# Optimization experiments

Hardware: AMD Instinct MI355X
Metric: run time of the kernel (lower is better)

Reference implementation:

```python
import jax, jax.numpy as jnp
import numpy as np

D = 2048
H = 16
DH = D // H  # 128
B = 512
EPS = 1e-5


def _layernorm(x, g, b):
    m = jnp.mean(x, axis=-1, keepdims=True)
    v = jnp.mean((x - m) ** 2, axis=-1, keepdims=True)
    return (x - m) * jax.lax.rsqrt(v + EPS) * g + b


def setup_inputs() -> dict:
    key = jax.random.key(0)
    ks = jax.random.split(key, 16)
    s_in = 1.0 / np.sqrt(D)
    s_ff = 1.0 / np.sqrt(4 * D)
    return {
        "x": jax.random.normal(ks[0], (B, D), jnp.float32),
        # per-head q/k/v projections, stacked over heads: [H, D, DH]
        "Wq": jax.random.uniform(ks[1], (H, D, DH), jnp.float32, -s_in, s_in),
        "bq": jax.random.uniform(ks[2], (H, DH), jnp.float32, -s_in, s_in),
        "Wk": jax.random.uniform(ks[3], (H, D, DH), jnp.float32, -s_in, s_in),
        "bk": jax.random.uniform(ks[4], (H, DH), jnp.float32, -s_in, s_in),
        "Wv": jax.random.uniform(ks[5], (H, D, DH), jnp.float32, -s_in, s_in),
        "bv": jax.random.uniform(ks[6], (H, DH), jnp.float32, -s_in, s_in),
        "Wo": jax.random.uniform(ks[7], (D, D), jnp.float32, -s_in, s_in),
        "bo": jax.random.uniform(ks[8], (D,), jnp.float32, -s_in, s_in),
        "W1": jax.random.uniform(ks[9], (D, 4 * D), jnp.float32, -s_in, s_in),
        "b1": jax.random.uniform(ks[10], (4 * D,), jnp.float32, -s_in, s_in),
        "W2": jax.random.uniform(ks[11], (4 * D, D), jnp.float32, -s_ff, s_ff),
        "b2": jax.random.uniform(ks[12], (D,), jnp.float32, -s_ff, s_ff),
        "g1": jnp.ones((D,), jnp.float32),
        "be1": jnp.zeros((D,), jnp.float32),
        "g2": jnp.ones((D,), jnp.float32),
        "be2": jnp.zeros((D,), jnp.float32),
    }


def reference(x, Wq, bq, Wk, bk, Wv, bv, Wo, bo, W1, b1, W2, b2, g1, be1, g2, be2):
    # --- pre-norm attention branch ---
    h = _layernorm(x, g1, be1)                       # [B, D]
    q = jnp.einsum('bd,hde->bhe', h, Wq) + bq        # [B, H, DH]
    k = jnp.einsum('bd,hde->bhe', h, Wk) + bk
    v = jnp.einsum('bd,hde->bhe', h, Wv) + bv
    # outer-product 'attention' per sample: [B, H, DH, DH]
    attn = q[..., :, None] * k[..., None, :] / jnp.sqrt(jnp.float32(DH))
    attn = jax.nn.softmax(attn, axis=-1)
    o = jnp.einsum('bhij,bhj->bhi', attn, v)         # [B, H, DH]
    o = o.reshape(x.shape[0], H * DH)                # concat over heads
    x = x + o @ Wo + bo
    # --- pre-norm FFN branch ---
    h2 = _layernorm(x, g2, be2)
    x = x + jax.nn.relu(h2 @ W1 + b1) @ W2 + b2
    return x
```

## Files before the change

### kernel.cpp

```cpp
#include <hip/hip_runtime.h>
#include <hip/hip_bf16.h>
#include <math.h>


#define DDIM 2048
#define HHEADS 16
#define DHEAD 128
#define BROWS 512
#define LN_EPS 1e-5f

typedef __bf16 bf16x8_t __attribute__((ext_vector_type(8)));
typedef float f32x4_t __attribute__((ext_vector_type(4)));

#define GLD16(gptr, lptr)                                                     \
    __builtin_amdgcn_global_load_lds(                                         \
        (const __attribute__((address_space(1))) void*)(gptr),                \
        (__attribute__((address_space(3))) void*)(lptr), 16, 0, 0)

__global__ __launch_bounds__(256) void ln_kernel(const float* __restrict__ x,
                                                 const float* __restrict__ g,
                                                 const float* __restrict__ b,
                                                 __bf16* __restrict__ out) {
    const int row = blockIdx.x;
    const int tid = threadIdx.x;
    const float4* x4 = (const float4*)(x + (size_t)row * DDIM);
    float4 a = x4[2 * tid];
    float4 c = x4[2 * tid + 1];
    float s  = a.x + a.y + a.z + a.w + c.x + c.y + c.z + c.w;
    float s2 = a.x*a.x + a.y*a.y + a.z*a.z + a.w*a.w
             + c.x*c.x + c.y*c.y + c.z*c.z + c.w*c.w;
    #pragma unroll
    for (int off = 32; off > 0; off >>= 1) {
        s  += __shfl_down(s, off);
        s2 += __shfl_down(s2, off);
    }
    __shared__ float ps[4], ps2[4];
    __shared__ float mean_s, rstd_s;
    const int lane = tid & 63, w = tid >> 6;
    if (lane == 0) { ps[w] = s; ps2[w] = s2; }
    __syncthreads();
    if (tid == 0) {
        float S  = ps[0] + ps[1] + ps[2] + ps[3];
        float S2 = ps2[0] + ps2[1] + ps2[2] + ps2[3];
        float m  = S * (1.0f / DDIM);
        float var = S2 * (1.0f / DDIM) - m * m;
        mean_s = m;
        rstd_s = rsqrtf(var + LN_EPS);
    }
    __syncthreads();
    const float m = mean_s, r = rstd_s;
    const float4* g4 = (const float4*)g;
    const float4* b4 = (const float4*)b;
    float4 ga = g4[2 * tid], gb = g4[2 * tid + 1];
    float4 ba = b4[2 * tid], bb = b4[2 * tid + 1];
    bf16x8_t o;
    o[0] = (__bf16)((a.x - m) * r * ga.x + ba.x);
    o[1] = (__bf16)((a.y - m) * r * ga.y + ba.y);
    o[2] = (__bf16)((a.z - m) * r * ga.z + ba.z);
    o[3] = (__bf16)((a.w - m) * r * ga.w + ba.w);
    o[4] = (__bf16)((c.x - m) * r * gb.x + bb.x);
    o[5] = (__bf16)((c.y - m) * r * gb.y + bb.y);
    o[6] = (__bf16)((c.z - m) * r * gb.z + bb.z);
    o[7] = (__bf16)((c.w - m) * r * gb.w + bb.w);
    *(bf16x8_t*)(out + (size_t)row * DDIM + tid * 8) = o;
}

__global__ __launch_bounds__(256) void transpose_kernel(
    const float* __restrict__ src, __bf16* __restrict__ dst, int R, int C) {
    __shared__ float tile[64][65];
    const size_t bofs = (size_t)blockIdx.z * R * C;
    src += bofs;
    dst += bofs;
    const int c0 = blockIdx.x * 64, r0 = blockIdx.y * 64;
    const int t = threadIdx.x;
    const int rr = t >> 4, cc = (t & 15) * 4;
    #pragma unroll
    for (int p = 0; p < 4; p++) {
        const float4 v =
            *(const float4*)(src + (size_t)(r0 + rr + 16 * p) * C + c0 + cc);
        tile[rr + 16 * p][cc]     = v.x;
        tile[rr + 16 * p][cc + 1] = v.y;
        tile[rr + 16 * p][cc + 2] = v.z;
        tile[rr + 16 * p][cc + 3] = v.w;
    }
    __syncthreads();
    const int slot = t & 7;
    #pragma unroll
    for (int p = 0; p < 2; p++) {
        const int c = (t >> 3) + 32 * p;
        bf16x8_t o;
        #pragma unroll
        for (int j = 0; j < 8; j++)
            o[j] = (__bf16)tile[slot * 8 + j][c];
        *(bf16x8_t*)(dst + (size_t)(c0 + c) * R + r0 + slot * 8) = o;
    }
}

__global__ __launch_bounds__(256) void transpose_qkv_kernel(
    const float* __restrict__ Wq, const float* __restrict__ Wk,
    const float* __restrict__ Wv, __bf16* __restrict__ dstall) {
    __shared__ float tile[64][65];
    const int z = blockIdx.z, which = z >> 4, hd = z & 15;
    const float* src = (which == 0) ? Wq : (which == 1) ? Wk : Wv;
    src += (size_t)hd * DDIM * DHEAD;
    __bf16* dst = dstall + (size_t)which * DDIM * DDIM + (size_t)hd * DDIM * DHEAD;
    const int R = DDIM, C = DHEAD;
    const int c0 = blockIdx.x * 64, r0 = blockIdx.y * 64;
    const int t = threadIdx.x;
    const int rr = t >> 4, cc = (t & 15) * 4;
    #pragma unroll
    for (int p = 0; p < 4; p++) {
        const float4 v =
            *(const float4*)(src + (size_t)(r0 + rr + 16 * p) * C + c0 + cc);
        tile[rr + 16 * p][cc]     = v.x;
        tile[rr + 16 * p][cc + 1] = v.y;
        tile[rr + 16 * p][cc + 2] = v.z;
        tile[rr + 16 * p][cc + 3] = v.w;
    }
    __syncthreads();
    const int slot = t & 7;
    #pragma unroll
    for (int p = 0; p < 2; p++) {
        const int c = (t >> 3) + 32 * p;
        bf16x8_t o;
        #pragma unroll
        for (int j = 0; j < 8; j++)
            o[j] = (__bf16)tile[slot * 8 + j][c];
        *(bf16x8_t*)(dst + (size_t)(c0 + c) * R + r0 + slot * 8) = o;
    }
}

template <int DEPTH, int SPLITZ, int OUT_BF16, int RELU, int RES, int BIAS3>
__global__ __launch_bounds__(512) void gemm_bt(
    const __bf16* __restrict__ A, int K,
    const __bf16* __restrict__ Bt,
    const float* __restrict__ bias, const float* __restrict__ biasB,
    const float* __restrict__ biasC,
    const float* __restrict__ Res,
    void* __restrict__ Cout, int N) {
    constexpr int TM = 128, TN = 128;
    constexpr int STG = (TM + TN) * 64;
    __shared__ __align__(16) __bf16 smem[DEPTH * STG];

    const int tid = threadIdx.x;
    const int w = tid >> 6, lane = tid & 63;
    const int m0 = blockIdx.y * TM, n0 = blockIdx.x * TN;

    const int Kloc = K / SPLITZ;
    const int kb = blockIdx.z * Kloc;
    const int NK = Kloc / 64;

    constexpr int NT = (TM + TN) / 8;
    constexpr int NI = NT / 8;

    const int srow = lane >> 3;
    const int sslot = (lane & 7) ^ srow;

    const __bf16* srcs[NI];
    int toff[NI];
    #pragma unroll
    for (int i = 0; i < NI; i++) {
        const int t = w + 8 * i;
        toff[i] = t * 512;
        const int r = t * 8 + srow;
        srcs[i] = (r < TM)
                      ? A + (size_t)(m0 + r) * K + kb + sslot * 8
                      : Bt + (size_t)(n0 + r - TM) * K + kb + sslot * 8;
    }

    constexpr int MI = 4, NJ = 4;
    const int wg = w & 3, kh = w >> 2;
    const int wm = (wg >> 1) * 64, wn = (wg & 1) * 64;
    const int fm = lane & 15, quad = lane >> 4;
    const int f7 = fm & 7;

    const int sl = ((kh * 4 + quad) ^ f7) * 16;
    int aoff[MI], boff[NJ];
    #pragma unroll
    for (int i = 0; i < MI; i++)
        aoff[i] = (wm + 16 * i + fm) * 128 + sl;
    #pragma unroll
    for (int j = 0; j < NJ; j++)
        boff[j] = (TM + wn + 16 * j + fm) * 128 + sl;

    f32x4_t acc[MI][NJ] = {};

    #pragma unroll
    for (int d = 0; d < DEPTH; d++)
        #pragma unroll
        for (int i = 0; i < NI; i++)
            GLD16(srcs[i] + d * 64, smem + d * STG + toff[i]);

    for (int ks = 0; ks < NK; ks++) {
        const char* st = (const char*)smem + (ks % DEPTH) * (STG * 2);
        asm volatile("s_waitcnt vmcnt(%0)\n\ts_barrier"
                     :: "i"((DEPTH - 1) * NI) : "memory");

        bf16x8_t a[MI], b[NJ];
        #pragma unroll
        for (int i = 0; i < MI; i++)
            a[i] = *(const bf16x8_t*)(st + aoff[i]);
        #pragma unroll
        for (int j = 0; j < NJ; j++)
            b[j] = *(const bf16x8_t*)(st + boff[j]);
        #pragma unroll
        for (int i = 0; i < MI; i++)
            #pragma unroll
            for (int j = 0; j < NJ; j++)
                acc[i][j] = __builtin_amdgcn_mfma_f32_16x16x32_bf16(
                    a[i], b[j], acc[i][j], 0, 0, 0);

        asm volatile("s_waitcnt lgkmcnt(0)\n\ts_barrier" ::: "memory");
        if (ks + DEPTH < NK) {
            __bf16* dst = smem + (ks % DEPTH) * STG;
            #pragma unroll
            for (int i = 0; i < NI; i++)
                GLD16(srcs[i] + (size_t)(ks + DEPTH) * 64, dst + toff[i]);
        }
    }

    char* mrg = (char*)smem + wg * 16384;
    if (kh == 1) {
        #pragma unroll
        for (int i = 0; i < MI; i++)
            #pragma unroll
            for (int j = 0; j < NJ; j++)
                *(f32x4_t*)(mrg + (((i * NJ + j) * 64) + lane) * 16) = acc[i][j];
    }
    __syncthreads();
    if (kh == 1) return;
    #pragma unroll
    for (int i = 0; i < MI; i++)
        #pragma unroll
        for (int j = 0; j < NJ; j++) {
            const f32x4_t p = *(const f32x4_t*)(mrg + (((i * NJ + j) * 64) + lane) * 16);
            acc[i][j][0] += p[0]; acc[i][j][1] += p[1];
            acc[i][j][2] += p[2]; acc[i][j][3] += p[3];
        }

    if (SPLITZ > 1) {
        float* P = (float*)Cout + (size_t)blockIdx.z * (gridDim.y * TM) * N;
        #pragma unroll
        for (int i = 0; i < MI; i++)
            #pragma unroll
            for (int j = 0; j < NJ; j++) {
                const int col = n0 + wn + 16 * j + fm;
                #pragma unroll
                for (int r = 0; r < 4; r++) {
                    const int row = m0 + wm + 16 * i + quad * 4 + r;
                    P[(size_t)row * N + col] = acc[i][j][r];
                }
            }
    } else {
        const float* bp = bias;
        if (BIAS3) {
            const int seg = n0 >> 11;
            bp = (seg == 0) ? bias : (seg == 1) ? biasB : biasC;
        }
        #pragma unroll
        for (int i = 0; i < MI; i++)
            #pragma unroll
            for (int j = 0; j < NJ; j++) {
                const int col = n0 + wn + 16 * j + fm;
                const float bcol = BIAS3 ? bp[col & 2047] : bp[col];
                #pragma unroll
                for (int r = 0; r < 4; r++) {
                    const int row = m0 + wm + 16 * i + quad * 4 + r;
                    float val = acc[i][j][r] + bcol;
                    if (RES) val += Res[(size_t)row * N + col];
                    if (RELU) val = fmaxf(val, 0.0f);
                    if (OUT_BF16)
                        ((__bf16*)Cout)[(size_t)row * N + col] = (__bf16)val;
                    else
                        ((float*)Cout)[(size_t)row * N + col] = val;
                }
            }
    }
}

template <int NS>
__global__ __launch_bounds__(256) void reduce_splitk(
    const float* __restrict__ part, const float* __restrict__ Res,
    const float* __restrict__ bias, float* __restrict__ out) {
    const int idx = blockIdx.x * 256 + threadIdx.x;
    const float4 b4 = ((const float4*)bias)[idx & 511];
    float4 r = ((const float4*)Res)[idx];
    #pragma unroll
    for (int s = 0; s < NS; s++) {
        const float4 p = ((const float4*)part)[(size_t)s * 262144 + idx];
        r.x += p.x; r.y += p.y; r.z += p.z; r.w += p.w;
    }
    r.x += b4.x; r.y += b4.y; r.z += b4.z; r.w += b4.w;
    ((float4*)out)[idx] = r;
}

template <int NS>
__global__ __launch_bounds__(256) void reduce_ln_kernel(
    const float* __restrict__ part, const float* __restrict__ x,
    const float* __restrict__ bo, const float* __restrict__ g,
    const float* __restrict__ be, float* __restrict__ x1,
    __bf16* __restrict__ h2) {
    const int row = blockIdx.x;
    const int tid = threadIdx.x;
    const size_t rbase = (size_t)row * DDIM;
    float v[8];
    #pragma unroll
    for (int p = 0; p < 2; p++) {
        const int c = tid * 8 + p * 4;
        float4 r = *(const float4*)(x + rbase + c);
        const float4 b4 = *(const float4*)(bo + c);
        r.x += b4.x; r.y += b4.y; r.z += b4.z; r.w += b4.w;
        #pragma unroll
        for (int s = 0; s < NS; s++) {
            const float4 q = *(const float4*)(part + (size_t)s * BROWS * DDIM + rbase + c);
            r.x += q.x; r.y += q.y; r.z += q.z; r.w += q.w;
        }
        *(float4*)(x1 + rbase + c) = r;
        v[p * 4 + 0] = r.x; v[p * 4 + 1] = r.y; v[p * 4 + 2] = r.z; v[p * 4 + 3] = r.w;
    }
    float s = 0.f, s2 = 0.f;
    #pragma unroll
    for (int i = 0; i < 8; i++) { s += v[i]; s2 += v[i] * v[i]; }
    #pragma unroll
    for (int off = 32; off > 0; off >>= 1) {
        s  += __shfl_down(s, off);
        s2 += __shfl_down(s2, off);
    }
    __shared__ float ps[4], ps2[4];
    __shared__ float mean_s, rstd_s;
    const int lane = tid & 63, wv = tid >> 6;
    if (lane == 0) { ps[wv] = s; ps2[wv] = s2; }
    __syncthreads();
    if (tid == 0) {
        float S  = ps[0] + ps[1] + ps[2] + ps[3];
        float S2 = ps2[0] + ps2[1] + ps2[2] + ps2[3];
        float m  = S * (1.0f / DDIM);
        float var = S2 * (1.0f / DDIM) - m * m;
        mean_s = m;
        rstd_s = rsqrtf(var + LN_EPS);
    }
    __syncthreads();
    const float m = mean_s, r = rstd_s;
    const float4* g4 = (const float4*)g;
    const float4* b4 = (const float4*)be;
    float4 ga = g4[2 * tid], gb = g4[2 * tid + 1];
    float4 ba = b4[2 * tid], bb = b4[2 * tid + 1];
    bf16x8_t o;
    o[0] = (__bf16)((v[0] - m) * r * ga.x + ba.x);
    o[1] = (__bf16)((v[1] - m) * r * ga.y + ba.y);
    o[2] = (__bf16)((v[2] - m) * r * ga.z + ba.z);
    o[3] = (__bf16)((v[3] - m) * r * ga.w + ba.w);
    o[4] = (__bf16)((v[4] - m) * r * gb.x + bb.x);
    o[5] = (__bf16)((v[5] - m) * r * gb.y + bb.y);
    o[6] = (__bf16)((v[6] - m) * r * gb.z + bb.z);
    o[7] = (__bf16)((v[7] - m) * r * gb.w + bb.w);
    *(bf16x8_t*)(h2 + rbase + tid * 8) = o;
}

__global__ __launch_bounds__(128) void attn_kernel(
    const __bf16* __restrict__ qkv, __bf16* __restrict__ o) {
    const int bh = blockIdx.x;
    const int b = bh >> 4, h = bh & 15;
    const size_t base = (size_t)b * (3 * DDIM) + h * DHEAD;
    const int tid = threadIdx.x;
    __shared__ float ks[DHEAD], vs[DHEAD];
    ks[tid] = (float)qkv[base + DDIM + tid];
    vs[tid] = (float)qkv[base + 2 * DDIM + tid];
    __syncthreads();
    const float a = (float)qkv[base + tid] * 0.08838834764831845f;
    float den = 0.0f, num = 0.0f;
    #pragma unroll 8
    for (int j = 0; j < DHEAD; j++) {
        float e = __expf(a * ks[j]);
        den += e;
        num += e * vs[j];
    }
    o[(size_t)b * DDIM + h * DHEAD + tid] = (__bf16)(num / den);
}

extern "C" void kernel_launch(void* const* d_in, const int* in_sizes, int n_in,
                              void* d_out, int out_size, void* d_ws, size_t ws_size,
                              hipStream_t stream) {
    const float* x   = (const float*)d_in[0];
    const float* Wq  = (const float*)d_in[1];
    const float* bq  = (const float*)d_in[2];
    const float* Wk  = (const float*)d_in[3];
    const float* bk  = (const float*)d_in[4];
    const float* Wv  = (const float*)d_in[5];
    const float* bv  = (const float*)d_in[6];
    const float* Wo  = (const float*)d_in[7];
    const float* bo  = (const float*)d_in[8];
    const float* W1  = (const float*)d_in[9];
    const float* b1  = (const float*)d_in[10];
    const float* W2  = (const float*)d_in[11];
    const float* b2  = (const float*)d_in[12];
    const float* g1  = (const float*)d_in[13];
    const float* be1 = (const float*)d_in[14];
    const float* g2  = (const float*)d_in[15];
    const float* be2 = (const float*)d_in[16];
    float* out = (float*)d_out;

    char* base = (char*)d_ws;
    __bf16* bt_qkv = (__bf16*)(base + 32768);
    char*   slotA  = base + 32768 + 25165824;
    char*   slotB  = slotA + 33554432;
    __bf16* h   = (__bf16*)(slotB + 0);
    __bf16* qkv = (__bf16*)(slotB + 2097152);
    __bf16* ob  = (__bf16*)(slotB + 8388608);
    float*  woP = (float*)(slotB + 10485760);
    float*  w2P = (float*)(slotB + 0);
    float*  x1  = (float*)((char*)bt_qkv + 0);
    __bf16* h2  = (__bf16*)((char*)bt_qkv + 4194304);
    __bf16* t   = (__bf16*)((char*)bt_qkv + 6291456);
    __bf16* Wot = (__bf16*)slotA;
    __bf16* W1t = (__bf16*)slotB;
    __bf16* W2t = (__bf16*)slotA;

    transpose_qkv_kernel<<<dim3(2, 32, 48), 256, 0, stream>>>(Wq, Wk, Wv, bt_qkv);
    transpose_kernel<<<dim3(32, 32, 1), 256, 0, stream>>>(Wo, Wot, DDIM, DDIM);

    ln_kernel<<<BROWS, 256, 0, stream>>>(x, g1, be1, h);

    gemm_bt<3, 1, 1, 0, 0, 1><<<dim3(48, 4), 512, 0, stream>>>(
        h, DDIM, bt_qkv, bq, bk, bv, nullptr, qkv, 3 * DDIM);

    attn_kernel<<<BROWS * HHEADS, 128, 0, stream>>>(qkv, ob);

    gemm_bt<3, 4, 0, 0, 0, 0><<<dim3(16, 4, 4), 512, 0, stream>>>(
        ob, DDIM, Wot, nullptr, nullptr, nullptr, nullptr, woP, DDIM);
    reduce_ln_kernel<4><<<BROWS, 256, 0, stream>>>(woP, x, bo, g2, be2, x1, h2);

    transpose_kernel<<<dim3(128, 32, 1), 256, 0, stream>>>(W1, W1t, DDIM, 4 * DDIM);
    transpose_kernel<<<dim3(32, 128, 1), 256, 0, stream>>>(W2, W2t, 4 * DDIM, DDIM);

    gemm_bt<3, 1, 1, 1, 0, 0><<<dim3(64, 4), 512, 0, stream>>>(
        h2, DDIM, W1t, b1, nullptr, nullptr, nullptr, t, 4 * DDIM);

    gemm_bt<3, 4, 0, 0, 0, 0><<<dim3(16, 4, 4), 512, 0, stream>>>(
        t, 4 * DDIM, W2t, nullptr, nullptr, nullptr, nullptr, w2P, DDIM);
    reduce_splitk<4><<<1024, 256, 0, stream>>>(w2P, x1, b2, out);
}
```

Baseline: 351.8 us.

## Deepen GEMM pipeline, issue prefetch before MFMA, remap blocks per XCD

```diff
diff --git a/kernel.cpp b/kernel.cpp
--- a/kernel.cpp
+++ b/kernel.cpp
@@ -130,7 +130,7 @@
     }
 }
 
-template <int DEPTH, int SPLITZ, int OUT_BF16, int RELU, int RES, int BIAS3>
+template <int SPLITZ, int OUT_BF16, int RELU, int RES, int BIAS3>
 __global__ __launch_bounds__(512) void gemm_bt(
     const __bf16* __restrict__ A, int K,
     const __bf16* __restrict__ Bt,
@@ -138,16 +138,27 @@
     const float* __restrict__ biasC,
     const float* __restrict__ Res,
     void* __restrict__ Cout, int N) {
-    constexpr int TM = 128, TN = 128;
+    constexpr int TM = 128, TN = 128, DEPTH = 4;
     constexpr int STG = (TM + TN) * 64;
     __shared__ __align__(16) __bf16 smem[DEPTH * STG];
 
     const int tid = threadIdx.x;
     const int w = tid >> 6, lane = tid & 63;
-    const int m0 = blockIdx.y * TM, n0 = blockIdx.x * TN;
+
+    const int gx = gridDim.x, gy = gridDim.y, gz = gridDim.z;
+    {
+    }
+    int l = blockIdx.x + gx * (blockIdx.y + gy * blockIdx.z);
+    const int xcd = l & 7;
+    int i0 = l >> 3;
+    const int by = i0 % gy; i0 /= gy;
+    const int bz = i0 % gz; i0 /= gz;
+    const int bx = xcd * (gx >> 3) + i0;
+
+    const int m0 = by * TM, n0 = bx * TN;
 
     const int Kloc = K / SPLITZ;
-    const int kb = blockIdx.z * Kloc;
+    const int kb = bz * Kloc;
     const int NK = Kloc / 64;
 
     constexpr int NT = (TM + TN) / 8;
@@ -193,8 +204,21 @@
 
     for (int ks = 0; ks < NK; ks++) {
         const char* st = (const char*)smem + (ks % DEPTH) * (STG * 2);
-        asm volatile("s_waitcnt vmcnt(%0)\n\ts_barrier"
-                     :: "i"((DEPTH - 1) * NI) : "memory");
+        if (ks < NK - 2)
+            asm volatile("s_waitcnt vmcnt(%0)\n\ts_barrier"
+                         :: "i"((DEPTH - 2) * NI) : "memory");
+        else if (ks == NK - 2)
+            asm volatile("s_waitcnt vmcnt(%0)\n\ts_barrier"
+                         :: "i"(NI) : "memory");
+        else
+            asm volatile("s_waitcnt vmcnt(0)\n\ts_barrier" ::: "memory");
+
+        if (ks >= 1 && ks + DEPTH - 1 < NK) {
+            __bf16* dst = smem + ((ks - 1) % DEPTH) * STG;
+            #pragma unroll
+            for (int i = 0; i < NI; i++)
+                GLD16(srcs[i] + (size_t)(ks + DEPTH - 1) * 64, dst + toff[i]);
+        }
 
         bf16x8_t a[MI], b[NJ];
         #pragma unroll
@@ -203,23 +227,18 @@
         #pragma unroll
         for (int j = 0; j < NJ; j++)
             b[j] = *(const bf16x8_t*)(st + boff[j]);
+        __builtin_amdgcn_s_setprio(1);
         #pragma unroll
         for (int i = 0; i < MI; i++)
             #pragma unroll
             for (int j = 0; j < NJ; j++)
                 acc[i][j] = __builtin_amdgcn_mfma_f32_16x16x32_bf16(
                     a[i], b[j], acc[i][j], 0, 0, 0);
-
-        asm volatile("s_waitcnt lgkmcnt(0)\n\ts_barrier" ::: "memory");
-        if (ks + DEPTH < NK) {
-            __bf16* dst = smem + (ks % DEPTH) * STG;
-            #pragma unroll
-            for (int i = 0; i < NI; i++)
-                GLD16(srcs[i] + (size_t)(ks + DEPTH) * 64, dst + toff[i]);
-        }
+        __builtin_amdgcn_s_setprio(0);
     }
 
     char* mrg = (char*)smem + wg * 16384;
+    __syncthreads();
     if (kh == 1) {
         #pragma unroll
         for (int i = 0; i < MI; i++)
@@ -239,7 +258,7 @@
         }
 
     if (SPLITZ > 1) {
-        float* P = (float*)Cout + (size_t)blockIdx.z * (gridDim.y * TM) * N;
+        float* P = (float*)Cout + (size_t)bz * (gy * TM) * N;
         #pragma unroll
         for (int i = 0; i < MI; i++)
             #pragma unroll
@@ -421,22 +440,22 @@
 
     ln_kernel<<<BROWS, 256, 0, stream>>>(x, g1, be1, h);
 
-    gemm_bt<3, 1, 1, 0, 0, 1><<<dim3(48, 4), 512, 0, stream>>>(
+    gemm_bt<1, 1, 0, 0, 1><<<dim3(48, 4), 512, 0, stream>>>(
         h, DDIM, bt_qkv, bq, bk, bv, nullptr, qkv, 3 * DDIM);
 
     attn_kernel<<<BROWS * HHEADS, 128, 0, stream>>>(qkv, ob);
 
-    gemm_bt<3, 4, 0, 0, 0, 0><<<dim3(16, 4, 4), 512, 0, stream>>>(
+    gemm_bt<4, 0, 0, 0, 0><<<dim3(16, 4, 4), 512, 0, stream>>>(
         ob, DDIM, Wot, nullptr, nullptr, nullptr, nullptr, woP, DDIM);
     reduce_ln_kernel<4><<<BROWS, 256, 0, stream>>>(woP, x, bo, g2, be2, x1, h2);
 
     transpose_kernel<<<dim3(128, 32, 1), 256, 0, stream>>>(W1, W1t, DDIM, 4 * DDIM);
     transpose_kernel<<<dim3(32, 128, 1), 256, 0, stream>>>(W2, W2t, 4 * DDIM, DDIM);
 
-    gemm_bt<3, 1, 1, 1, 0, 0><<<dim3(64, 4), 512, 0, stream>>>(
+    gemm_bt<1, 1, 1, 0, 0><<<dim3(64, 4), 512, 0, stream>>>(
         h2, DDIM, W1t, b1, nullptr, nullptr, nullptr, t, 4 * DDIM);
 
-    gemm_bt<3, 4, 0, 0, 0, 0><<<dim3(16, 4, 4), 512, 0, stream>>>(
+    gemm_bt<4, 0, 0, 0, 0><<<dim3(16, 4, 4), 512, 0, stream>>>(
         t, 4 * DDIM, W2t, nullptr, nullptr, nullptr, nullptr, w2P, DDIM);
     reduce_splitk<4><<<1024, 256, 0, stream>>>(w2P, x1, b2, out);
 }
```

After: 351.6 us. No clear change (-0.1%).
